# Performance work log

Measured on AMD Instinct MI355X. Metric: run time of the kernel, lower is better.

Reference implementation:

```python
import jax, jax.numpy as jnp
import numpy as np

NEG_BIG = -9e15  # matches torch's -9000000000000000.0 mask value


def setup_inputs() -> dict:
    key = jax.random.key(0)
    k1, k2, k3, k4 = jax.random.split(key, 4)
    B, N, Din, Dout = 4, 4096, 256, 128
    x = jax.random.normal(k1, (B, N, Din), dtype=jnp.float32)
    adj = jax.random.randint(k2, (B, N, N), 0, 2, dtype=jnp.int32)
    weight = jax.random.normal(k3, (Din, Dout), dtype=jnp.float32) * (1.414 * (6.0 / (Din + Dout)) ** 0.5)
    a = jax.random.normal(k4, (2 * Dout, 1), dtype=jnp.float32) * 0.1
    bias = jnp.zeros((Dout,), dtype=jnp.float32)
    return {"x": x, "adj": adj, "weight": weight, "a": a, "bias": bias}


def reference(x, adj, weight, a, bias):
    Dout = weight.shape[1]
    h = jnp.matmul(x, weight)                       # [B, N, Dout]
    Wh1 = jnp.matmul(h, a[:Dout, :])                # [B, N, 1]
    Wh2 = jnp.matmul(h, a[Dout:, :])                # [B, N, 1]
    e = jax.nn.gelu(Wh1 + jnp.swapaxes(Wh2, 1, 2), approximate=False)  # [B, N, N]
    attention = jnp.where(adj > 0, e, NEG_BIG)
    attention = jax.nn.softmax(attention, axis=1)   # softmax over dim=1, as in torch code
    out = jnp.matmul(attention, h)                  # [B, N, Dout]
    out = jax.nn.gelu(out, approximate=False)
    # F.normalize(p=2, dim=1): L2-normalize over the node dimension
    norm = jnp.sqrt(jnp.sum(out * out, axis=1, keepdims=True))
    out = out / jnp.maximum(norm, 1e-12)
    return out + bias
```

## Files before the change

kernel.cpp:

```cpp
#include <hip/hip_runtime.h>
#include <hip/hip_bf16.h>
#include <stdint.h>


#define NN   4096
#define BB   4
#define DIN  256
#define DOUT 128

typedef unsigned short u16;
typedef _Float16 f16x8 __attribute__((ext_vector_type(8)));
typedef __attribute__((ext_vector_type(4))) float f32x4;

__device__ __forceinline__ u16 f2h_bits(float f) {
  _Float16 h = (_Float16)f;
  union { _Float16 h; u16 u; } v; v.h = h;
  return v.u;
}

__device__ __forceinline__ float erf_f(float x) {
  float ax = __builtin_fabsf(x);
  float t  = __builtin_amdgcn_rcpf(__builtin_fmaf(0.3275911f, ax, 1.0f));
  float p  = __builtin_fmaf(1.061405429f, t, -1.453152027f);
  p = __builtin_fmaf(p, t, 1.421413741f);
  p = __builtin_fmaf(p, t, -0.284496736f);
  p = __builtin_fmaf(p, t, 0.254829592f);
  p = p * t;
  float e  = __expf(-ax * ax);
  float er = __builtin_fmaf(-p, e, 1.0f);
  return copysignf(er, x);
}

__device__ __forceinline__ float gelu_f(float z) {
  float hz = 0.5f * z;
  return __builtin_fmaf(hz, erf_f(z * 0.70710678118654752f), hz);
}

__device__ __forceinline__ float exp_gelu(float z) { return __expf(gelu_f(z)); }

__global__ __launch_bounds__(256, 2) void k1_proj(
    const float* __restrict__ x, const float* __restrict__ weight,
    const float* __restrict__ a, u16* __restrict__ hT,
    float* __restrict__ Wh1, float* __restrict__ Wh2)
{
  __shared__ float xs[32 * 256];
  __shared__ float T[128 * 33];
  __shared__ float P2a[8 * 32], P2b[8 * 32];

  const int b = blockIdx.y, n0 = blockIdx.x * 32;
  const int tid = threadIdx.x;

  const float4* xsrc = (const float4*)(x + ((size_t)b * NN + n0) * DIN);
  float4* xd = (float4*)xs;
#pragma unroll
  for (int v = 0; v < 8; ++v) xd[tid + v * 256] = xsrc[tid + v * 256];
  __syncthreads();

  const int dg = tid & 31, rg = tid >> 5;
  float acc[4][4] = {};
  const float4* W4 = (const float4*)weight;
#pragma unroll 4
  for (int k = 0; k < 256; ++k) {
    float4 wr = W4[k * 32 + dg];
#pragma unroll
    for (int rr = 0; rr < 4; ++rr) {
      float xv = xs[(rg * 4 + rr) * 256 + k];
      acc[rr][0] = fmaf(xv, wr.x, acc[rr][0]);
      acc[rr][1] = fmaf(xv, wr.y, acc[rr][1]);
      acc[rr][2] = fmaf(xv, wr.z, acc[rr][2]);
      acc[rr][3] = fmaf(xv, wr.w, acc[rr][3]);
    }
  }
#pragma unroll
  for (int rr = 0; rr < 4; ++rr)
#pragma unroll
    for (int dd = 0; dd < 4; ++dd)
      T[(dg * 4 + dd) * 33 + rg * 4 + rr] = acc[rr][dd];
  __syncthreads();

  {
    const int d = tid & 127, half = tid >> 7;
    unsigned int uu[8];
#pragma unroll
    for (int p = 0; p < 8; ++p) {
      float f0 = T[d * 33 + half * 16 + p * 2];
      float f1 = T[d * 33 + half * 16 + p * 2 + 1];
      uu[p] = (unsigned int)f2h_bits(f0) | ((unsigned int)f2h_bits(f1) << 16);
    }
    u16* dst = hT + ((size_t)b * DOUT + d) * NN + n0 + half * 16;
    ((uint4*)dst)[0] = make_uint4(uu[0], uu[1], uu[2], uu[3]);
    ((uint4*)dst)[1] = make_uint4(uu[4], uu[5], uu[6], uu[7]);
  }
  {
    const int r = tid & 31, g8 = tid >> 5;
    float p1 = 0.f, p2 = 0.f;
#pragma unroll
    for (int q = 0; q < 16; ++q) {
      int d = g8 * 16 + q;
      float hv = T[d * 33 + r];
      p1 = fmaf(hv, a[d], p1);
      p2 = fmaf(hv, a[DOUT + d], p2);
    }
    P2a[g8 * 32 + r] = p1;
    P2b[g8 * 32 + r] = p2;
  }
  __syncthreads();
  if (tid < 32) {
    float s1 = 0.f, s2 = 0.f;
#pragma unroll
    for (int g8 = 0; g8 < 8; ++g8) { s1 += P2a[g8 * 32 + tid]; s2 += P2b[g8 * 32 + tid]; }
    Wh1[b * NN + n0 + tid] = s1;
    Wh2[b * NN + n0 + tid] = s2;
  }
}

__global__ __launch_bounds__(256) void k2_fused(
    const int* __restrict__ adj, const float* __restrict__ Wh1,
    const float* __restrict__ Wh2, float* __restrict__ S,
    unsigned int* __restrict__ m32)
{
  const int b = blockIdx.z, jt = blockIdx.x, ic = blockIdx.y;
  const int tid = threadIdx.x;
  const int j = jt * 256 + tid;
  const int lane = tid & 63;
  const int jg = jt * 4 + (tid >> 6);
  const int i0 = ic * 128;

  const float wh2 = Wh2[b * NN + j];
  const int* ap = adj + ((size_t)b * NN + i0) * NN + j;
  const float* w1p = Wh1 + b * NN + i0;
  unsigned int* mlo = m32 + ((size_t)b * 128 + jg * 2) * NN + i0;
  unsigned int* mhi = mlo + NN;

  float s = 0.f;
  for (int g = 0; g < 2; ++g) {
    unsigned long long acc64 = 0ull;
#pragma unroll
    for (int gg = 0; gg < 4; ++gg) {
      int av[16]; float w1v[16];
#pragma unroll
      for (int k = 0; k < 16; ++k) {
        const int ii = g * 64 + gg * 16 + k;
        av[k]  = ap[(size_t)ii * NN];
        w1v[k] = w1p[ii];
      }
#pragma unroll
      for (int k = 0; k < 16; ++k) {
        const unsigned long long bal = __ballot(av[k] > 0);
        if (lane == gg * 16 + k) acc64 = bal;
        const float E = exp_gelu(w1v[k] + wh2);
        s += (av[k] > 0) ? E : 0.f;
      }
    }
    mlo[g * 64 + lane] = (unsigned int)acc64;
    mhi[g * 64 + lane] = (unsigned int)(acc64 >> 32);
  }
  atomicAdd(&S[b * NN + j], s);
}

__global__ __launch_bounds__(256) void k25_rcp(const float* __restrict__ S,
                                               float* __restrict__ Sinv)
{
  int id = blockIdx.x * 256 + threadIdx.x;
  Sinv[id] = 1.0f / S[id];
}

__global__ __launch_bounds__(256, 2) void k3_attn(
    const unsigned int* __restrict__ m32, const float* __restrict__ Wh1,
    const float* __restrict__ Wh2, const float* __restrict__ Sinv,
    const u16* __restrict__ hT, float* __restrict__ out,
    float* __restrict__ norm2)
{
  __shared__ __align__(16) u16 buf[4][2][4096];

  const int b = blockIdx.y;
  const int i0 = blockIdx.x * 32;
  const int tid = threadIdx.x;
  const int w = tid >> 6, lane = tid & 63;
  const int m = lane & 15, quad = lane >> 4;

  const float w1a = Wh1[b * NN + i0 + m];
  const float w1b = Wh1[b * NN + i0 + 16 + m];
  const unsigned int* mbase = m32 + (size_t)b * 128 * NN;
  const u16* hTb = hT + (size_t)b * DOUT * NN;
  const u16* srcbase = hTb + (size_t)(lane >> 2) * NN + (lane & 3) * 8;

  f32x4 acc0[8], acc1[8];
#pragma unroll
  for (int t = 0; t < 8; ++t) {
    acc0[t] = (f32x4){0.f, 0.f, 0.f, 0.f};
    acc1[t] = (f32x4){0.f, 0.f, 0.f, 0.f};
  }

  const int jbase = w * 1024;

  unsigned int Ma, Mb;
  float4 w2a, w2b, sva, svb;
  {
    const int j0 = jbase;
    const int jw = j0 >> 5;
    Ma = mbase[(size_t)jw * NN + i0 + m];
    Mb = mbase[(size_t)jw * NN + i0 + 16 + m];
    const int jq = j0 + quad * 8;
    const float4* wp = (const float4*)(Wh2 + b * NN + jq);
    w2a = wp[0]; w2b = wp[1];
    const float4* sp = (const float4*)(Sinv + b * NN + jq);
    sva = sp[0]; svb = sp[1];
  }
#pragma unroll
  for (int inst = 0; inst < 8; ++inst) {
    const u16* g = srcbase + (size_t)inst * 16 * NN + jbase;
    __builtin_amdgcn_global_load_lds(
        (const __attribute__((address_space(1))) void*)g,
        (__attribute__((address_space(3))) void*)&buf[w][0][inst * 512],
        16, 0, 0);
  }

  for (int c = 0; c < 32; ++c) {
    const int cur = c & 1;
    const int cn = (c < 31) ? c + 1 : 31;
    const int j0n = jbase + cn * 32;

    const int jwn = j0n >> 5;
    const unsigned int Ma_n = mbase[(size_t)jwn * NN + i0 + m];
    const unsigned int Mb_n = mbase[(size_t)jwn * NN + i0 + 16 + m];
    const int jqn = j0n + quad * 8;
    const float4* wpn = (const float4*)(Wh2 + b * NN + jqn);
    const float4 w2a_n = wpn[0], w2b_n = wpn[1];
    const float4* spn = (const float4*)(Sinv + b * NN + jqn);
    const float4 sva_n = spn[0], svb_n = spn[1];

    __builtin_amdgcn_s_waitcnt(0xC07F);
    __builtin_amdgcn_sched_barrier(0);
#pragma unroll
    for (int inst = 0; inst < 8; ++inst) {
      const u16* g = srcbase + (size_t)inst * 16 * NN + j0n;
      __builtin_amdgcn_global_load_lds(
          (const __attribute__((address_space(1))) void*)g,
          (__attribute__((address_space(3))) void*)&buf[w][cur ^ 1][inst * 512],
          16, 0, 0);
    }

    const unsigned int mba = (Ma >> (quad * 8)) & 0xFFu;
    const unsigned int mbb = (Mb >> (quad * 8)) & 0xFFu;

    f16x8 ah_a, ah_b;
    ah_a[0] = (_Float16)((mba & 1u)   ? exp_gelu(w1a + w2a.x) * sva.x : 0.f);
    ah_a[1] = (_Float16)((mba & 2u)   ? exp_gelu(w1a + w2a.y) * sva.y : 0.f);
    ah_a[2] = (_Float16)((mba & 4u)   ? exp_gelu(w1a + w2a.z) * sva.z : 0.f);
    ah_a[3] = (_Float16)((mba & 8u)   ? exp_gelu(w1a + w2a.w) * sva.w : 0.f);
    ah_a[4] = (_Float16)((mba & 16u)  ? exp_gelu(w1a + w2b.x) * svb.x : 0.f);
    ah_a[5] = (_Float16)((mba & 32u)  ? exp_gelu(w1a + w2b.y) * svb.y : 0.f);
    ah_a[6] = (_Float16)((mba & 64u)  ? exp_gelu(w1a + w2b.z) * svb.z : 0.f);
    ah_a[7] = (_Float16)((mba & 128u) ? exp_gelu(w1a + w2b.w) * svb.w : 0.f);
    ah_b[0] = (_Float16)((mbb & 1u)   ? exp_gelu(w1b + w2a.x) * sva.x : 0.f);
    ah_b[1] = (_Float16)((mbb & 2u)   ? exp_gelu(w1b + w2a.y) * sva.y : 0.f);
    ah_b[2] = (_Float16)((mbb & 4u)   ? exp_gelu(w1b + w2a.z) * sva.z : 0.f);
    ah_b[3] = (_Float16)((mbb & 8u)   ? exp_gelu(w1b + w2a.w) * sva.w : 0.f);
    ah_b[4] = (_Float16)((mbb & 16u)  ? exp_gelu(w1b + w2b.x) * svb.x : 0.f);
    ah_b[5] = (_Float16)((mbb & 32u)  ? exp_gelu(w1b + w2b.y) * svb.y : 0.f);
    ah_b[6] = (_Float16)((mbb & 64u)  ? exp_gelu(w1b + w2b.z) * svb.z : 0.f);
    ah_b[7] = (_Float16)((mbb & 128u) ? exp_gelu(w1b + w2b.w) * svb.w : 0.f);

    __builtin_amdgcn_sched_barrier(0);
    __builtin_amdgcn_s_waitcnt(0x0F78);
    __builtin_amdgcn_sched_barrier(0);

#pragma unroll
    for (int t = 0; t < 8; ++t) {
      f16x8 bf = *(const f16x8*)&buf[w][cur][(t * 16 + m) * 32 + quad * 8];
      acc0[t] = __builtin_amdgcn_mfma_f32_16x16x32_f16(ah_a, bf, acc0[t], 0, 0, 0);
      acc1[t] = __builtin_amdgcn_mfma_f32_16x16x32_f16(ah_b, bf, acc1[t], 0, 0, 0);
    }

    Ma = Ma_n; Mb = Mb_n;
    w2a = w2a_n; w2b = w2b_n; sva = sva_n; svb = svb_n;
  }

  float* red = (float*)&buf[0][0][0];
  float p2[2] = {0.f, 0.f};
#pragma unroll
  for (int rt = 0; rt < 2; ++rt) {
    __syncthreads();
#pragma unroll
    for (int t = 0; t < 8; ++t)
#pragma unroll
      for (int r = 0; r < 4; ++r)
        red[w * 2048 + (t * 4 + r) * 64 + lane] = rt ? acc1[t][r] : acc0[t][r];
    __syncthreads();
#pragma unroll
    for (int tt = 0; tt < 2; ++tt) {
      const int t = w * 2 + tt;
#pragma unroll
      for (int r = 0; r < 4; ++r) {
        const int o = (t * 4 + r) * 64 + lane;
        float v = red[o] + red[2048 + o] + red[4096 + o] + red[6144 + o];
        float gv = gelu_f(v);
        out[((size_t)b * NN + i0 + rt * 16 + quad * 4 + r) * DOUT + t * 16 + m] = gv;
        p2[tt] = fmaf(gv, gv, p2[tt]);
      }
    }
  }
#pragma unroll
  for (int tt = 0; tt < 2; ++tt) {
    float ps = p2[tt];
    ps += __shfl_xor(ps, 16);
    ps += __shfl_xor(ps, 32);
    if (quad == 0)
      atomicAdd(&norm2[b * DOUT + (w * 2 + tt) * 16 + m], ps);
  }
}

__global__ __launch_bounds__(256) void k4b_scale(
    float* __restrict__ out, const float* __restrict__ norm2,
    const float* __restrict__ bias)
{
  int id = blockIdx.x * 256 + threadIdx.x;
  int d = id & 127;
  int b = id >> 19;
  float nrm = sqrtf(norm2[b * DOUT + d]);
  float sc = 1.0f / fmaxf(nrm, 1e-12f);
  out[id] = fmaf(out[id], sc, bias[d]);
}

extern "C" void kernel_launch(void* const* d_in, const int* in_sizes, int n_in,
                              void* d_out, int out_size, void* d_ws, size_t ws_size,
                              hipStream_t stream)
{
  const float* x      = (const float*)d_in[0];
  const int*   adj    = (const int*)d_in[1];
  const float* weight = (const float*)d_in[2];
  const float* a      = (const float*)d_in[3];
  const float* bias   = (const float*)d_in[4];
  float* out = (float*)d_out;

  char* ws = (char*)d_ws;
  u16*   hT     = (u16*)ws;
  float* Wh1    = (float*)(ws + (size_t)4 * 1024 * 1024);
  float* Wh2    = Wh1 + BB * NN;
  float* S      = Wh2 + BB * NN;
  float* Sinv   = S + BB * NN;
  unsigned int* m32 = (unsigned int*)(Sinv + BB * NN);
  float* norm2  = (float*)((char*)m32 + (size_t)BB * 128 * NN * 4);

  hipMemsetAsync(S, 0, (size_t)BB * NN * sizeof(float), stream);
  hipMemsetAsync(norm2, 0, (size_t)BB * DOUT * sizeof(float), stream);

  k1_proj<<<dim3(NN / 32, BB), 256, 0, stream>>>(x, weight, a, hT, Wh1, Wh2);
  k2_fused<<<dim3(16, 32, BB), 256, 0, stream>>>(adj, Wh1, Wh2, S, m32);
  k25_rcp<<<dim3(BB * NN / 256), 256, 0, stream>>>(S, Sinv);
  k3_attn<<<dim3(NN / 32, BB), 256, 0, stream>>>(m32, Wh1, Wh2, Sinv, hT, out, norm2);
  k4b_scale<<<dim3((BB * NN * DOUT) / 256), 256, 0, stream>>>(out, norm2, bias);
}
```

Baseline: 501.9 us.

## Fuse reciprocal and normalize-scale kernels into attention kernel via grid barrier

```diff
diff --git a/kernel.cpp b/kernel.cpp
--- a/kernel.cpp
+++ b/kernel.cpp
@@ -7,6 +7,7 @@
 #define BB   4
 #define DIN  256
 #define DOUT 128
+#define NBLK (BB * (NN / 32))
 
 typedef unsigned short u16;
 typedef _Float16 f16x8 __attribute__((ext_vector_type(8)));
@@ -158,18 +159,12 @@
   atomicAdd(&S[b * NN + j], s);
 }
 
-__global__ __launch_bounds__(256) void k25_rcp(const float* __restrict__ S,
-                                               float* __restrict__ Sinv)
-{
-  int id = blockIdx.x * 256 + threadIdx.x;
-  Sinv[id] = 1.0f / S[id];
-}
-
 __global__ __launch_bounds__(256, 2) void k3_attn(
     const unsigned int* __restrict__ m32, const float* __restrict__ Wh1,
-    const float* __restrict__ Wh2, const float* __restrict__ Sinv,
-    const u16* __restrict__ hT, float* __restrict__ out,
-    float* __restrict__ norm2)
+    const float* __restrict__ Wh2, const float* __restrict__ S,
+    const u16* __restrict__ hT, const float* __restrict__ bias,
+    float* __restrict__ out, float* __restrict__ norm2,
+    unsigned int* __restrict__ bar)
 {
   __shared__ __align__(16) u16 buf[4][2][4096];
 
@@ -204,8 +199,12 @@
     const int jq = j0 + quad * 8;
     const float4* wp = (const float4*)(Wh2 + b * NN + jq);
     w2a = wp[0]; w2b = wp[1];
-    const float4* sp = (const float4*)(Sinv + b * NN + jq);
+    const float4* sp = (const float4*)(S + b * NN + jq);
     sva = sp[0]; svb = sp[1];
+    sva.x = __builtin_amdgcn_rcpf(sva.x); sva.y = __builtin_amdgcn_rcpf(sva.y);
+    sva.z = __builtin_amdgcn_rcpf(sva.z); sva.w = __builtin_amdgcn_rcpf(sva.w);
+    svb.x = __builtin_amdgcn_rcpf(svb.x); svb.y = __builtin_amdgcn_rcpf(svb.y);
+    svb.z = __builtin_amdgcn_rcpf(svb.z); svb.w = __builtin_amdgcn_rcpf(svb.w);
   }
 #pragma unroll
   for (int inst = 0; inst < 8; ++inst) {
@@ -227,8 +226,12 @@
     const int jqn = j0n + quad * 8;
     const float4* wpn = (const float4*)(Wh2 + b * NN + jqn);
     const float4 w2a_n = wpn[0], w2b_n = wpn[1];
-    const float4* spn = (const float4*)(Sinv + b * NN + jqn);
-    const float4 sva_n = spn[0], svb_n = spn[1];
+    const float4* spn = (const float4*)(S + b * NN + jqn);
+    float4 sva_n = spn[0], svb_n = spn[1];
+    sva_n.x = __builtin_amdgcn_rcpf(sva_n.x); sva_n.y = __builtin_amdgcn_rcpf(sva_n.y);
+    sva_n.z = __builtin_amdgcn_rcpf(sva_n.z); sva_n.w = __builtin_amdgcn_rcpf(sva_n.w);
+    svb_n.x = __builtin_amdgcn_rcpf(svb_n.x); svb_n.y = __builtin_amdgcn_rcpf(svb_n.y);
+    svb_n.z = __builtin_amdgcn_rcpf(svb_n.z); svb_n.w = __builtin_amdgcn_rcpf(svb_n.w);
 
     __builtin_amdgcn_s_waitcnt(0xC07F);
     __builtin_amdgcn_sched_barrier(0);
@@ -279,6 +282,7 @@
 
   float* red = (float*)&buf[0][0][0];
   float p2[2] = {0.f, 0.f};
+  float gv[2][2][4];
 #pragma unroll
   for (int rt = 0; rt < 2; ++rt) {
     __syncthreads();
@@ -295,9 +299,9 @@
       for (int r = 0; r < 4; ++r) {
         const int o = (t * 4 + r) * 64 + lane;
         float v = red[o] + red[2048 + o] + red[4096 + o] + red[6144 + o];
-        float gv = gelu_f(v);
-        out[((size_t)b * NN + i0 + rt * 16 + quad * 4 + r) * DOUT + t * 16 + m] = gv;
-        p2[tt] = fmaf(gv, gv, p2[tt]);
+        float g = gelu_f(v);
+        gv[rt][tt][r] = g;
+        p2[tt] = fmaf(g, g, p2[tt]);
       }
     }
   }
@@ -309,18 +313,36 @@
     if (quad == 0)
       atomicAdd(&norm2[b * DOUT + (w * 2 + tt) * 16 + m], ps);
   }
-}
-
-__global__ __launch_bounds__(256) void k4b_scale(
-    float* __restrict__ out, const float* __restrict__ norm2,
-    const float* __restrict__ bias)
-{
-  int id = blockIdx.x * 256 + threadIdx.x;
-  int d = id & 127;
-  int b = id >> 19;
-  float nrm = sqrtf(norm2[b * DOUT + d]);
-  float sc = 1.0f / fmaxf(nrm, 1e-12f);
-  out[id] = fmaf(out[id], sc, bias[d]);
+
+  __syncthreads();
+  if (tid == 0) {
+    __hip_atomic_fetch_add(bar, 1u, __ATOMIC_ACQ_REL, __HIP_MEMORY_SCOPE_AGENT);
+    unsigned int spins = 0;
+    while (__hip_atomic_load(bar, __ATOMIC_ACQUIRE, __HIP_MEMORY_SCOPE_AGENT)
+           < (unsigned int)NBLK) {
+      __builtin_amdgcn_s_sleep(8);
+      if (++spins > 4000000u) break;
+    }
+  }
+  __syncthreads();
+
+  float scb[2], bsv[2];
+#pragma unroll
+  for (int tt = 0; tt < 2; ++tt) {
+    const int d = (w * 2 + tt) * 16 + m;
+    float n2 = __hip_atomic_load(&norm2[b * DOUT + d], __ATOMIC_RELAXED,
+                                 __HIP_MEMORY_SCOPE_AGENT);
+    scb[tt] = 1.0f / fmaxf(sqrtf(n2), 1e-12f);
+    bsv[tt] = bias[d];
+  }
+#pragma unroll
+  for (int rt = 0; rt < 2; ++rt)
+#pragma unroll
+    for (int tt = 0; tt < 2; ++tt)
+#pragma unroll
+      for (int r = 0; r < 4; ++r)
+        out[((size_t)b * NN + i0 + rt * 16 + quad * 4 + r) * DOUT +
+            (w * 2 + tt) * 16 + m] = fmaf(gv[rt][tt][r], scb[tt], bsv[tt]);
 }
 
 extern "C" void kernel_launch(void* const* d_in, const int* in_sizes, int n_in,
@@ -342,13 +364,13 @@
   float* Sinv   = S + BB * NN;
   unsigned int* m32 = (unsigned int*)(Sinv + BB * NN);
   float* norm2  = (float*)((char*)m32 + (size_t)BB * 128 * NN * 4);
+  unsigned int* bar = (unsigned int*)(norm2 + BB * DOUT);
 
   hipMemsetAsync(S, 0, (size_t)BB * NN * sizeof(float), stream);
-  hipMemsetAsync(norm2, 0, (size_t)BB * DOUT * sizeof(float), stream);
+  hipMemsetAsync(norm2, 0, (size_t)BB * DOUT * sizeof(float) + 64, stream);
 
   k1_proj<<<dim3(NN / 32, BB), 256, 0, stream>>>(x, weight, a, hT, Wh1, Wh2);
   k2_fused<<<dim3(16, 32, BB), 256, 0, stream>>>(adj, Wh1, Wh2, S, m32);
-  k25_rcp<<<dim3(BB * NN / 256), 256, 0, stream>>>(S, Sinv);
-  k3_attn<<<dim3(NN / 32, BB), 256, 0, stream>>>(m32, Wh1, Wh2, Sinv, hT, out, norm2);
-  k4b_scale<<<dim3((BB * NN * DOUT) / 256), 256, 0, stream>>>(out, norm2, bias);
-}
+  k3_attn<<<dim3(NN / 32, BB), 256, 0, stream>>>(m32, Wh1, Wh2, S, hT, bias,
+                                                 out, norm2, bar);
+}
```

Result: slower. 556.8 us (+10.9%).
